# Performance work log

Measured on AMD Instinct MI355X. Metric: run time of the kernel, lower is better.

## Reference

```python
import jax, jax.numpy as jnp
import numpy as np

INITIAL_RADIUS = 1.0


def setup_inputs() -> dict:
    key = jax.random.key(0)
    k1, k2, k3 = jax.random.split(key, 3)
    B, N, S = 4, 8192, 2048
    xyz = jax.random.normal(k1, (B, 3, N), dtype=jnp.float32)
    sparse_xyz = jax.random.normal(k2, (B, 3, S), dtype=jnp.float32)
    sparse_flow = jax.random.normal(k3, (B, 3, S), dtype=jnp.float32)
    return {"xyz": xyz, "sparse_xyz": sparse_xyz, "sparse_flow": sparse_flow,
            "resol_factor": 1}


def reference(xyz, sparse_xyz, sparse_flow, resol_factor):
    # xyz: [B,3,N], sparse_xyz/sparse_flow: [B,3,S]
    radius = INITIAL_RADIUS * resol_factor
    x = jnp.transpose(xyz, (0, 2, 1))          # [B,N,3] dense query points
    y = jnp.transpose(sparse_xyz, (0, 2, 1))   # [B,S,3] sparse support points
    f = jnp.transpose(sparse_flow, (0, 2, 1))  # [B,S,3] sparse flow values
    B, S, _ = y.shape
    w = jnp.ones((B, S, 1), dtype=x.dtype)     # uniform sample weights

    # squared pairwise distances D2[b,n,s] = ||x_bn - y_bs||^2
    x2 = jnp.sum(x * x, axis=-1, keepdims=True)            # [B,N,1]
    y2 = jnp.sum(y * y, axis=-1)[:, None, :]               # [B,1,S]
    xy = jnp.einsum('bnd,bsd->bns', x, y)                  # [B,N,S]
    d2 = x2 + y2 - 2.0 * xy

    # Gaussian Nadaraya-Watson kernel weights
    k = jnp.exp(-d2 / (radius * radius))                   # [B,N,S]

    num = jnp.einsum('bns,bsd->bnd', k, f * w)             # [B,N,3]
    den = jnp.einsum('bns,bsd->bnd', k, w)                 # [B,N,1]
    dense = num / den                                      # [B,N,3]
    return jnp.transpose(dense, (0, 2, 1))                 # [B,3,N]
```

## Files before the change

kernel.cpp:

```cpp
#include <hip/hip_runtime.h>


typedef float v2f __attribute__((ext_vector_type(2)));

constexpr int B_ = 4, N_ = 8192, S_ = 2048;
constexpr int BLOCK = 256, PPT = 8;
constexpr int PTS_PER_BLOCK = BLOCK * PPT;
constexpr int NBPB = N_ / PTS_PER_BLOCK;
constexpr int NB = B_ * NBPB;
constexpr int BN = B_ * N_;
constexpr float LOG2E = 1.4426950408889634f;

#define PK_FMA(d, a, b, c) \
    asm("v_pk_fma_f32 %0, %1, %2, %3" : "=v"(d) : "v"(a), "v"(b), "v"(c))
#define PK_FMA_ACC(acc, a, b) \
    asm("v_pk_fma_f32 %0, %1, %2, %0" : "+v"(acc) : "v"(a), "v"(b))
#define PK_ADD_ACC(acc, a) \
    asm("v_pk_add_f32 %0, %1, %0" : "+v"(acc) : "v"(a))

template <int CHUNK>
__global__ __launch_bounds__(BLOCK, 2) void uf2_main(
    const float* __restrict__ xyz,
    const float* __restrict__ sxyz,
    const float* __restrict__ sflow,
    const int* __restrict__ resol,
    float4* __restrict__ part)
{
    constexpr int TP = CHUNK / 2;
    __shared__ float4 AXY[TP];
    __shared__ float4 AZW[TP];
    __shared__ float4 FXY[TP];
    __shared__ v2f    FZ2[TP];

    const int nb = blockIdx.x % NB;
    const int sc = blockIdx.x / NB;
    const int b  = nb / NBPB;
    const int n0 = (nb % NBPB) * PTS_PER_BLOCK;
    const int s0 = sc * CHUNK;

    const float r = (float)resol[0];
    const float inv_r2 = 1.0f / (r * r);
    const float c2 = 2.0f * inv_r2 * LOG2E;
    const float cy = -inv_r2 * LOG2E;

    const float* yb = sxyz  + b * 3 * S_;
    const float* fb = sflow + b * 3 * S_;
    for (int tp = threadIdx.x; tp < TP; tp += BLOCK) {
        const int s = s0 + 2 * tp;
        const float yx0 = yb[s],          yx1 = yb[s + 1];
        const float yy0 = yb[S_ + s],     yy1 = yb[S_ + s + 1];
        const float yz0 = yb[2 * S_ + s], yz1 = yb[2 * S_ + s + 1];
        const float fx0 = fb[s],          fx1 = fb[s + 1];
        const float fy0 = fb[S_ + s],     fy1 = fb[S_ + s + 1];
        const float fz0 = fb[2 * S_ + s], fz1 = fb[2 * S_ + s + 1];
        AXY[tp] = make_float4(c2 * yx0, c2 * yx1, c2 * yy0, c2 * yy1);
        AZW[tp] = make_float4(c2 * yz0, c2 * yz1,
                              cy * (yx0 * yx0 + yy0 * yy0 + yz0 * yz0),
                              cy * (yx1 * yx1 + yy1 * yy1 + yz1 * yz1));
        FXY[tp] = make_float4(fx0, fx1, fy0, fy1);
        FZ2[tp] = (v2f){fz0, fz1};
    }
    __syncthreads();

    const float* xb = xyz + b * 3 * N_;
    v2f px2[PPT], py2[PPT], pz2[PPT];
    v2f acx[PPT], acy[PPT], acz[PPT], acw[PPT];
#pragma unroll
    for (int p = 0; p < PPT; ++p) {
        const int n = n0 + threadIdx.x + p * BLOCK;
        const float x = xb[n], y = xb[N_ + n], z = xb[2 * N_ + n];
        px2[p] = (v2f){x, x}; py2[p] = (v2f){y, y}; pz2[p] = (v2f){z, z};
        acx[p] = (v2f){0.f, 0.f}; acy[p] = (v2f){0.f, 0.f};
        acz[p] = (v2f){0.f, 0.f}; acw[p] = (v2f){0.f, 0.f};
    }

#pragma unroll 2
    for (int tp = 0; tp < TP; ++tp) {
        const float4 axy = AXY[tp];
        const float4 azw = AZW[tp];
        const float4 fxy = FXY[tp];
        const v2f fz2 = FZ2[tp];
        const v2f ax2 = (v2f){axy.x, axy.y}, ay2 = (v2f){axy.z, axy.w};
        const v2f az2 = (v2f){azw.x, azw.y}, aw2 = (v2f){azw.z, azw.w};
        const v2f fx2 = (v2f){fxy.x, fxy.y}, fy2 = (v2f){fxy.z, fxy.w};
#pragma unroll
        for (int p = 0; p < PPT; ++p) {
            v2f e2;
            PK_FMA(e2, pz2[p], az2, aw2);
            PK_FMA_ACC(e2, py2[p], ay2);
            PK_FMA_ACC(e2, px2[p], ax2);
            v2f k2;
            k2.x = __builtin_amdgcn_exp2f(e2.x);
            k2.y = __builtin_amdgcn_exp2f(e2.y);
            PK_FMA_ACC(acx[p], k2, fx2);
            PK_FMA_ACC(acy[p], k2, fy2);
            PK_FMA_ACC(acz[p], k2, fz2);
            PK_ADD_ACC(acw[p], k2);
        }
    }

#pragma unroll
    for (int p = 0; p < PPT; ++p) {
        const int g = b * N_ + n0 + threadIdx.x + p * BLOCK;
        part[(size_t)sc * BN + g] = make_float4(
            acx[p].x + acx[p].y, acy[p].x + acy[p].y,
            acz[p].x + acz[p].y, acw[p].x + acw[p].y);
    }
}

__global__ __launch_bounds__(BLOCK) void uf2_combine(
    const float4* __restrict__ part, float* __restrict__ out, int SC)
{
    const int g = blockIdx.x * BLOCK + threadIdx.x;
    float4 s = make_float4(0.f, 0.f, 0.f, 0.f);
    for (int c = 0; c < SC; ++c) {
        const float4 p = part[(size_t)c * BN + g];
        s.x += p.x; s.y += p.y; s.z += p.z; s.w += p.w;
    }
    const float inv = 1.0f / s.w;
    const int b = g >> 13;
    const int n = g & (N_ - 1);
    float* ob = out + b * 3 * N_;
    ob[n]          = s.x * inv;
    ob[N_ + n]     = s.y * inv;
    ob[2 * N_ + n] = s.z * inv;
}

__global__ __launch_bounds__(BLOCK, 1) void uf2_fused(
    const float* __restrict__ xyz,
    const float* __restrict__ sxyz,
    const float* __restrict__ sflow,
    const int* __restrict__ resol,
    float* __restrict__ out)
{
    constexpr int FPPT = 4;
    constexpr int PTS = BLOCK * FPPT;
    __shared__ float4 As[S_];
    __shared__ float4 Fs[S_];

    const int nb = blockIdx.x;
    const int b  = nb / (N_ / PTS);
    const int n0 = (nb % (N_ / PTS)) * PTS;

    const float r = (float)resol[0];
    const float inv_r2 = 1.0f / (r * r);
    const float c2 = 2.0f * inv_r2 * LOG2E;
    const float cy = -inv_r2 * LOG2E;

    const float* yb = sxyz  + b * 3 * S_;
    const float* fb = sflow + b * 3 * S_;
    for (int t = threadIdx.x; t < S_; t += BLOCK) {
        const float yx = yb[t], yy = yb[S_ + t], yz = yb[2 * S_ + t];
        const float fx = fb[t], fy = fb[S_ + t], fz = fb[2 * S_ + t];
        As[t] = make_float4(c2 * yx, c2 * yy, c2 * yz,
                            cy * (yx * yx + yy * yy + yz * yz));
        Fs[t] = make_float4(fx, fy, fz, 0.0f);
    }
    __syncthreads();

    const float* xb = xyz + b * 3 * N_;
    float px[FPPT], py[FPPT], pz[FPPT];
    float4 acc[FPPT];
#pragma unroll
    for (int p = 0; p < FPPT; ++p) {
        const int n = n0 + threadIdx.x + p * BLOCK;
        px[p] = xb[n]; py[p] = xb[N_ + n]; pz[p] = xb[2 * N_ + n];
        acc[p] = make_float4(0.f, 0.f, 0.f, 0.f);
    }
#pragma unroll 4
    for (int t = 0; t < S_; ++t) {
        const float4 a = As[t];
        const float4 f = Fs[t];
#pragma unroll
        for (int p = 0; p < FPPT; ++p) {
            float e = fmaf(pz[p], a.z, a.w);
            e = fmaf(py[p], a.y, e);
            e = fmaf(px[p], a.x, e);
            const float k = __builtin_amdgcn_exp2f(e);
            acc[p].x = fmaf(k, f.x, acc[p].x);
            acc[p].y = fmaf(k, f.y, acc[p].y);
            acc[p].z = fmaf(k, f.z, acc[p].z);
            acc[p].w += k;
        }
    }
#pragma unroll
    for (int p = 0; p < FPPT; ++p) {
        const int n = n0 + threadIdx.x + p * BLOCK;
        const float inv = 1.0f / acc[p].w;
        float* ob = out + b * 3 * N_;
        ob[n]          = acc[p].x * inv;
        ob[N_ + n]     = acc[p].y * inv;
        ob[2 * N_ + n] = acc[p].z * inv;
    }
}

extern "C" void kernel_launch(void* const* d_in, const int* in_sizes, int n_in,
                              void* d_out, int out_size, void* d_ws, size_t ws_size,
                              hipStream_t stream)
{
    const float* xyz   = (const float*)d_in[0];
    const float* sxyz  = (const float*)d_in[1];
    const float* sflow = (const float*)d_in[2];
    const int*   resol = (const int*)d_in[3];
    float* out = (float*)d_out;
    float4* part = (float4*)d_ws;

    const size_t per_chunk = (size_t)BN * sizeof(float4);
    int SC = 32;
    while (SC > 1 && (size_t)SC * per_chunk > ws_size) SC >>= 1;

    if ((size_t)SC * per_chunk > ws_size) {
        uf2_fused<<<dim3(BN / 1024), dim3(BLOCK), 0, stream>>>(
            xyz, sxyz, sflow, resol, out);
        return;
    }

    dim3 grid(NB * SC), blk(BLOCK);
    switch (SC) {
        case 32: uf2_main<S_ / 32><<<grid, blk, 0, stream>>>(xyz, sxyz, sflow, resol, part); break;
        case 16: uf2_main<S_ / 16><<<grid, blk, 0, stream>>>(xyz, sxyz, sflow, resol, part); break;
        case 8:  uf2_main<S_ / 8 ><<<grid, blk, 0, stream>>>(xyz, sxyz, sflow, resol, part); break;
        case 4:  uf2_main<S_ / 4 ><<<grid, blk, 0, stream>>>(xyz, sxyz, sflow, resol, part); break;
        case 2:  uf2_main<S_ / 2 ><<<grid, blk, 0, stream>>>(xyz, sxyz, sflow, resol, part); break;
        default: uf2_main<S_     ><<<grid, blk, 0, stream>>>(xyz, sxyz, sflow, resol, part); break;
    }
    uf2_combine<<<dim3(BN / BLOCK), dim3(BLOCK), 0, stream>>>(part, out, SC);
}
```

Measured before the change: 34.71 us.

## Replace hardware exp2 with polynomial exp2, raise occupancy, halve S-split, unroll combine

```diff
diff --git a/kernel.cpp b/kernel.cpp
--- a/kernel.cpp
+++ b/kernel.cpp
@@ -11,6 +11,13 @@
 constexpr int BN = B_ * N_;
 constexpr float LOG2E = 1.4426950408889634f;
 
+constexpr float C5 = 1.535336188319500e-4f;
+constexpr float C4 = 1.339887440266574e-3f;
+constexpr float C3 = 9.618437357674640e-3f;
+constexpr float C2 = 5.550332471162809e-2f;
+constexpr float C1 = 2.402264791363012e-1f;
+constexpr float C0 = 6.931472028550421e-1f;
+
 #define PK_FMA(d, a, b, c) \
     asm("v_pk_fma_f32 %0, %1, %2, %3" : "=v"(d) : "v"(a), "v"(b), "v"(c))
 #define PK_FMA_ACC(acc, a, b) \
@@ -19,7 +26,7 @@
     asm("v_pk_add_f32 %0, %1, %0" : "+v"(acc) : "v"(a))
 
 template <int CHUNK>
-__global__ __launch_bounds__(BLOCK, 2) void uf2_main(
+__global__ __launch_bounds__(BLOCK, 4) void uf2_main(
     const float* __restrict__ xyz,
     const float* __restrict__ sxyz,
     const float* __restrict__ sflow,
@@ -74,28 +81,44 @@
         acz[p] = (v2f){0.f, 0.f}; acw[p] = (v2f){0.f, 0.f};
     }
 
+    const v2f c52 = (v2f){C5, C5}, c42 = (v2f){C4, C4}, c32 = (v2f){C3, C3};
+    const v2f c22 = (v2f){C2, C2}, c12 = (v2f){C1, C1}, c02 = (v2f){C0, C0};
+    const v2f one2 = (v2f){1.0f, 1.0f};
+
 #pragma unroll 2
     for (int tp = 0; tp < TP; ++tp) {
-        const float4 axy = AXY[tp];
-        const float4 azw = AZW[tp];
-        const float4 fxy = FXY[tp];
-        const v2f fz2 = FZ2[tp];
-        const v2f ax2 = (v2f){axy.x, axy.y}, ay2 = (v2f){axy.z, axy.w};
-        const v2f az2 = (v2f){azw.x, azw.y}, aw2 = (v2f){azw.z, azw.w};
-        const v2f fx2 = (v2f){fxy.x, fxy.y}, fy2 = (v2f){fxy.z, fxy.w};
+        const float4 a1 = AXY[tp];
+        const float4 a2 = AZW[tp];
+        const float4 f1 = FXY[tp];
+        const v2f    fz2 = FZ2[tp];
+        const v2f ax2 = (v2f){a1.x, a1.y}, ay2 = (v2f){a1.z, a1.w};
+        const v2f az2 = (v2f){a2.x, a2.y}, bi2 = (v2f){a2.z, a2.w};
+        const v2f fx2 = (v2f){f1.x, f1.y}, fy2 = (v2f){f1.z, f1.w};
 #pragma unroll
         for (int p = 0; p < PPT; ++p) {
             v2f e2;
-            PK_FMA(e2, pz2[p], az2, aw2);
+            PK_FMA(e2, pz2[p], az2, bi2);
             PK_FMA_ACC(e2, py2[p], ay2);
             PK_FMA_ACC(e2, px2[p], ax2);
+            const float fl0 = floorf(e2.x), fl1 = floorf(e2.y);
+            const v2f fl2 = (v2f){fl0, fl1};
+            const v2f f2 = e2 - fl2;
+            const int i0 = (int)fl0, i1 = (int)fl1;
+            v2f pp;
+            PK_FMA(pp, c52, f2, c42);
+            PK_FMA(pp, pp, f2, c32);
+            PK_FMA(pp, pp, f2, c22);
+            PK_FMA(pp, pp, f2, c12);
+            PK_FMA(pp, pp, f2, c02);
             v2f k2;
-            k2.x = __builtin_amdgcn_exp2f(e2.x);
-            k2.y = __builtin_amdgcn_exp2f(e2.y);
-            PK_FMA_ACC(acx[p], k2, fx2);
-            PK_FMA_ACC(acy[p], k2, fy2);
-            PK_FMA_ACC(acz[p], k2, fz2);
-            PK_ADD_ACC(acw[p], k2);
+            PK_FMA(k2, pp, f2, one2);
+            const float k0 = ldexpf(k2.x, i0);
+            const float k1 = ldexpf(k2.y, i1);
+            const v2f kk = (v2f){k0, k1};
+            PK_FMA_ACC(acx[p], kk, fx2);
+            PK_FMA_ACC(acy[p], kk, fy2);
+            PK_FMA_ACC(acz[p], kk, fz2);
+            PK_ADD_ACC(acw[p], kk);
         }
     }
 
@@ -112,18 +135,34 @@
     const float4* __restrict__ part, float* __restrict__ out, int SC)
 {
     const int g = blockIdx.x * BLOCK + threadIdx.x;
-    float4 s = make_float4(0.f, 0.f, 0.f, 0.f);
-    for (int c = 0; c < SC; ++c) {
+    float4 s0 = make_float4(0.f, 0.f, 0.f, 0.f);
+    float4 s1 = s0, s2 = s0, s3 = s0;
+    int c = 0;
+    for (; c + 4 <= SC; c += 4) {
+        const float4 p0 = part[(size_t)(c + 0) * BN + g];
+        const float4 p1 = part[(size_t)(c + 1) * BN + g];
+        const float4 p2 = part[(size_t)(c + 2) * BN + g];
+        const float4 p3 = part[(size_t)(c + 3) * BN + g];
+        s0.x += p0.x; s0.y += p0.y; s0.z += p0.z; s0.w += p0.w;
+        s1.x += p1.x; s1.y += p1.y; s1.z += p1.z; s1.w += p1.w;
+        s2.x += p2.x; s2.y += p2.y; s2.z += p2.z; s2.w += p2.w;
+        s3.x += p3.x; s3.y += p3.y; s3.z += p3.z; s3.w += p3.w;
+    }
+    for (; c < SC; ++c) {
         const float4 p = part[(size_t)c * BN + g];
-        s.x += p.x; s.y += p.y; s.z += p.z; s.w += p.w;
-    }
-    const float inv = 1.0f / s.w;
+        s0.x += p.x; s0.y += p.y; s0.z += p.z; s0.w += p.w;
+    }
+    const float sx = (s0.x + s1.x) + (s2.x + s3.x);
+    const float sy = (s0.y + s1.y) + (s2.y + s3.y);
+    const float sz = (s0.z + s1.z) + (s2.z + s3.z);
+    const float sw = (s0.w + s1.w) + (s2.w + s3.w);
+    const float inv = 1.0f / sw;
     const int b = g >> 13;
     const int n = g & (N_ - 1);
     float* ob = out + b * 3 * N_;
-    ob[n]          = s.x * inv;
-    ob[N_ + n]     = s.y * inv;
-    ob[2 * N_ + n] = s.z * inv;
+    ob[n]          = sx * inv;
+    ob[N_ + n]     = sy * inv;
+    ob[2 * N_ + n] = sz * inv;
 }
 
 __global__ __launch_bounds__(BLOCK, 1) void uf2_fused(
@@ -206,7 +245,7 @@
     float4* part = (float4*)d_ws;
 
     const size_t per_chunk = (size_t)BN * sizeof(float4);
-    int SC = 32;
+    int SC = 16;
     while (SC > 1 && (size_t)SC * per_chunk > ws_size) SC >>= 1;
 
     if ((size_t)SC * per_chunk > ws_size) {
@@ -217,7 +256,6 @@
 
     dim3 grid(NB * SC), blk(BLOCK);
     switch (SC) {
-        case 32: uf2_main<S_ / 32><<<grid, blk, 0, stream>>>(xyz, sxyz, sflow, resol, part); break;
         case 16: uf2_main<S_ / 16><<<grid, blk, 0, stream>>>(xyz, sxyz, sflow, resol, part); break;
         case 8:  uf2_main<S_ / 8 ><<<grid, blk, 0, stream>>>(xyz, sxyz, sflow, resol, part); break;
         case 4:  uf2_main<S_ / 4 ><<<grid, blk, 0, stream>>>(xyz, sxyz, sflow, resol, part); break;
```

Measured after the change: 79.66 us. +129.5%, slower.
